# Kernel tuning notes

Measured on AMD Instinct MI355X. Metric: run time of the kernel, lower is better.

Reference implementation:

```python
import jax, jax.numpy as jnp
import numpy as np

N_HEAD = 16

def setup_inputs() -> dict:
    key = jax.random.key(0)
    ks = jax.random.split(key, 5)
    B, T, D = 2, 2048, 1024
    BN = 1024  # bottleneck_dim
    s = 0.02
    return {
        "x": jax.random.normal(ks[0], (B, T, D), dtype=jnp.float32),
        "w_qkv": jax.random.normal(ks[1], (3 * BN, D), dtype=jnp.float32) * s,
        "b_qkv": jax.random.normal(ks[2], (3 * BN,), dtype=jnp.float32) * s,
        "w_proj": jax.random.normal(ks[3], (D, BN), dtype=jnp.float32) * s,
        "b_proj": jax.random.normal(ks[4], (D,), dtype=jnp.float32) * s,
        "top_k": 64,
    }

def reference(x, w_qkv, b_qkv, w_proj, b_proj, top_k):
    B, T, D = x.shape
    H = N_HEAD
    BN = w_qkv.shape[0] // 3
    Dh = BN // H
    # qkv projection; torch Linear: y = x @ W^T + b
    qkv = (x @ w_qkv.T + b_qkv).reshape(B, T, 3, H, Dh)
    q = jnp.moveaxis(qkv[:, :, 0], 1, 2)  # (B,H,T,Dh)
    k = jnp.moveaxis(qkv[:, :, 1], 1, 2)
    v = jnp.moveaxis(qkv[:, :, 2], 1, 2)
    att = jnp.einsum('bhqd,bhkd->bhqk', q, k) * (1.0 / np.sqrt(Dh).astype(np.float32))
    # SparseK mask: keep only top-k scores per query row, mask rest before softmax
    topv = jax.lax.top_k(att, top_k)[0]          # (B,H,T,top_k)
    thresh = topv[..., -1:]                      # kth largest per row
    att = jnp.where(att >= thresh, att, -jnp.inf)
    att = jax.nn.softmax(att, axis=-1)
    y = jnp.einsum('bhqk,bhkd->bhqd', att, v)    # (B,H,T,Dh)
    y = y.transpose(0, 2, 1, 3).reshape(B, T, BN)
    return y @ w_proj.T + b_proj
```

## Files before the change

### kernel.cpp

```cpp
#include <hip/hip_runtime.h>
#include <hip/hip_bf16.h>
#include <math.h>

#define Bz 2
#define Tz 2048
#define Dz 1024
#define Hz 16
#define DHz 64
#define BNz 1024
#define TOPKz 64
#define QBLK 16
#define CAND_MAX 176
#define BAND 8e-5f
#define SLO  -20.0f
#define SBINW 0.15625f
#define SBINR 6.4f
#define LDSB 40
#define HSTR 257

typedef __attribute__((ext_vector_type(8))) short bf16x8;
typedef __attribute__((ext_vector_type(4))) short s16x4;
typedef __attribute__((ext_vector_type(4))) float f32x4;

__device__ __forceinline__ short f2bf(float f) {
  unsigned u = __float_as_uint(f);
  return (short)((u + 0x7FFFu + ((u >> 16) & 1u)) >> 16);
}
__device__ __forceinline__ float bf2f(short b) {
  return __uint_as_float(((unsigned)(unsigned short)b) << 16);
}
__device__ __forceinline__ unsigned f2s(float f) {
  unsigned u = __float_as_uint(f);
  return (u & 0x80000000u) ? ~u : (u | 0x80000000u);
}
__device__ __forceinline__ float s2f(unsigned u) {
  return __uint_as_float((u & 0x80000000u) ? (u & 0x7FFFFFFFu) : ~u);
}

__global__ __launch_bounds__(256) void split3(
    const float* __restrict__ in, short* __restrict__ hh,
    short* __restrict__ mm, short* __restrict__ ll, int n4)
{
  int i = blockIdx.x * 256 + threadIdx.x;
  if (i >= n4) return;
  float4 v = ((const float4*)in)[i];
  float vv[4] = {v.x, v.y, v.z, v.w};
  s16x4 h4, m4, l4;
#pragma unroll
  for (int e = 0; e < 4; ++e) {
    short h = f2bf(vv[e]);
    float r1 = vv[e] - bf2f(h);
    short m = f2bf(r1);
    float r2 = r1 - bf2f(m);
    h4[e] = h; m4[e] = m; l4[e] = f2bf(r2);
  }
  ((s16x4*)hh)[i] = h4;
  ((s16x4*)mm)[i] = m4;
  ((s16x4*)ll)[i] = l4;
}

__global__ __launch_bounds__(256) void qkv_gemm_v2(
    const short* __restrict__ Axh, const short* __restrict__ Axm,
    const short* __restrict__ Axl, const short* __restrict__ Bwh,
    const short* __restrict__ Bwm, const short* __restrict__ Bwl,
    const float* __restrict__ bias,
    float* __restrict__ q32, float* __restrict__ k32,
    short* __restrict__ kbf, float* __restrict__ v32)
{
  __shared__ __align__(16) short Ah[128][LDSB];
  __shared__ __align__(16) short Am[128][LDSB];
  __shared__ __align__(16) short Al[128][LDSB];
  __shared__ __align__(16) short Bh[64][LDSB];
  __shared__ __align__(16) short Bm[64][LDSB];
  __shared__ __align__(16) short Bl[64][LDSB];

  const int tid = threadIdx.x;
  const int lane = tid & 63, wid = tid >> 6;
  const int m0 = blockIdx.y * 128, n0 = blockIdx.x * 64;
  const int bcol = lane & 15, lgrp = lane >> 4;

  f32x4 acch[2][4], accl[2][4];
#pragma unroll
  for (int ms = 0; ms < 2; ++ms)
#pragma unroll
    for (int nt = 0; nt < 4; ++nt) {
      acch[ms][nt] = (f32x4){0.f, 0.f, 0.f, 0.f};
      accl[ms][nt] = (f32x4){0.f, 0.f, 0.f, 0.f};
    }

  const int arow = tid >> 1, ak = (tid & 1) * 16;
  const int brow = tid >> 2, bk = (tid & 3) * 8;
  const size_t aoff = (size_t)(m0 + arow) * Dz + ak;
  const size_t boff = (size_t)(n0 + brow) * Dz + bk;

  for (int kt = 0; kt < Dz; kt += 32) {
    bf16x8 ah0 = *(const bf16x8*)(Axh + aoff + kt);
    bf16x8 ah1 = *(const bf16x8*)(Axh + aoff + kt + 8);
    bf16x8 am0 = *(const bf16x8*)(Axm + aoff + kt);
    bf16x8 am1 = *(const bf16x8*)(Axm + aoff + kt + 8);
    bf16x8 al0 = *(const bf16x8*)(Axl + aoff + kt);
    bf16x8 al1 = *(const bf16x8*)(Axl + aoff + kt + 8);
    bf16x8 bh8 = *(const bf16x8*)(Bwh + boff + kt);
    bf16x8 bm8 = *(const bf16x8*)(Bwm + boff + kt);
    bf16x8 bl8 = *(const bf16x8*)(Bwl + boff + kt);
    __syncthreads();
    *(bf16x8*)&Ah[arow][ak] = ah0;  *(bf16x8*)&Ah[arow][ak+8] = ah1;
    *(bf16x8*)&Am[arow][ak] = am0;  *(bf16x8*)&Am[arow][ak+8] = am1;
    *(bf16x8*)&Al[arow][ak] = al0;  *(bf16x8*)&Al[arow][ak+8] = al1;
    *(bf16x8*)&Bh[brow][bk] = bh8;
    *(bf16x8*)&Bm[brow][bk] = bm8;
    *(bf16x8*)&Bl[brow][bk] = bl8;
    __syncthreads();

    bf16x8 ahf[2], amf[2], alf[2];
#pragma unroll
    for (int ms = 0; ms < 2; ++ms) {
      int rr = wid*32 + ms*16 + bcol;
      ahf[ms] = *(const bf16x8*)&Ah[rr][lgrp*8];
      amf[ms] = *(const bf16x8*)&Am[rr][lgrp*8];
      alf[ms] = *(const bf16x8*)&Al[rr][lgrp*8];
    }
#pragma unroll
    for (int nt = 0; nt < 4; ++nt) {
      int nr = nt*16 + bcol;
      bf16x8 bh = *(const bf16x8*)&Bh[nr][lgrp*8];
      bf16x8 bm = *(const bf16x8*)&Bm[nr][lgrp*8];
      bf16x8 bl = *(const bf16x8*)&Bl[nr][lgrp*8];
#pragma unroll
      for (int ms = 0; ms < 2; ++ms) {
        acch[ms][nt] = __builtin_amdgcn_mfma_f32_16x16x32_bf16(ahf[ms], bh, acch[ms][nt], 0, 0, 0);
        accl[ms][nt] = __builtin_amdgcn_mfma_f32_16x16x32_bf16(ahf[ms], bm, accl[ms][nt], 0, 0, 0);
        accl[ms][nt] = __builtin_amdgcn_mfma_f32_16x16x32_bf16(amf[ms], bh, accl[ms][nt], 0, 0, 0);
        accl[ms][nt] = __builtin_amdgcn_mfma_f32_16x16x32_bf16(amf[ms], bm, accl[ms][nt], 0, 0, 0);
        accl[ms][nt] = __builtin_amdgcn_mfma_f32_16x16x32_bf16(ahf[ms], bl, accl[ms][nt], 0, 0, 0);
        accl[ms][nt] = __builtin_amdgcn_mfma_f32_16x16x32_bf16(alf[ms], bh, accl[ms][nt], 0, 0, 0);
      }
    }
  }

#pragma unroll
  for (int ms = 0; ms < 2; ++ms)
#pragma unroll
    for (int nt = 0; nt < 4; ++nt)
#pragma unroll
      for (int rv = 0; rv < 4; ++rv) {
        int m = m0 + wid*32 + ms*16 + lgrp*4 + rv;
        int n = n0 + nt*16 + bcol;
        double val = (double)acch[ms][nt][rv] + (double)accl[ms][nt][rv] + (double)bias[n];
        int bb = m >> 11;
        int t = m & 2047;
        if (n < BNz) {
          int h = n >> 6, d = n & 63;
          q32[(((size_t)(bb*Hz + h))*Tz + t)*DHz + d] = (float)val;
        } else if (n < 2*BNz) {
          int h = (n - BNz) >> 6, d = n & 63;
          size_t bh = (size_t)(bb*Hz + h);
          float vf = (float)val;
          k32[(bh*Tz + t)*DHz + d] = vf;
          kbf[(bh*Tz + t)*DHz + d] = f2bf(vf);
        } else {
          int h = (n - 2*BNz) >> 6, d = n & 63;
          v32[(((size_t)(bb*Hz + h))*Tz + t)*DHz + d] = (float)val;
        }
      }
}

__global__ __launch_bounds__(256) void proj_gemm_v2(
    const short* __restrict__ Ayh, const short* __restrict__ Aym,
    const short* __restrict__ Ayl, const short* __restrict__ Bwh,
    const short* __restrict__ Bwm, const short* __restrict__ Bwl,
    const float* __restrict__ bias, float* __restrict__ out)
{
  __shared__ __align__(16) short Ah[128][LDSB];
  __shared__ __align__(16) short Am[128][LDSB];
  __shared__ __align__(16) short Al[128][LDSB];
  __shared__ __align__(16) short Bh[64][LDSB];
  __shared__ __align__(16) short Bm[64][LDSB];
  __shared__ __align__(16) short Bl[64][LDSB];

  const int tid = threadIdx.x;
  const int lane = tid & 63, wid = tid >> 6;
  const int m0 = blockIdx.y * 128, n0 = blockIdx.x * 64;
  const int bcol = lane & 15, lgrp = lane >> 4;

  f32x4 acch[2][4], accl[2][4];
#pragma unroll
  for (int ms = 0; ms < 2; ++ms)
#pragma unroll
    for (int nt = 0; nt < 4; ++nt) {
      acch[ms][nt] = (f32x4){0.f, 0.f, 0.f, 0.f};
      accl[ms][nt] = (f32x4){0.f, 0.f, 0.f, 0.f};
    }

  const int arow = tid >> 1, ak = (tid & 1) * 16;
  const int brow = tid >> 2, bk = (tid & 3) * 8;
  const size_t aoff = (size_t)(m0 + arow) * Dz + ak;
  const size_t boff = (size_t)(n0 + brow) * Dz + bk;

  for (int kt = 0; kt < Dz; kt += 32) {
    bf16x8 ah0 = *(const bf16x8*)(Ayh + aoff + kt);
    bf16x8 ah1 = *(const bf16x8*)(Ayh + aoff + kt + 8);
    bf16x8 am0 = *(const bf16x8*)(Aym + aoff + kt);
    bf16x8 am1 = *(const bf16x8*)(Aym + aoff + kt + 8);
    bf16x8 al0 = *(const bf16x8*)(Ayl + aoff + kt);
    bf16x8 al1 = *(const bf16x8*)(Ayl + aoff + kt + 8);
    bf16x8 bh8 = *(const bf16x8*)(Bwh + boff + kt);
    bf16x8 bm8 = *(const bf16x8*)(Bwm + boff + kt);
    bf16x8 bl8 = *(const bf16x8*)(Bwl + boff + kt);
    __syncthreads();
    *(bf16x8*)&Ah[arow][ak] = ah0;  *(bf16x8*)&Ah[arow][ak+8] = ah1;
    *(bf16x8*)&Am[arow][ak] = am0;  *(bf16x8*)&Am[arow][ak+8] = am1;
    *(bf16x8*)&Al[arow][ak] = al0;  *(bf16x8*)&Al[arow][ak+8] = al1;
    *(bf16x8*)&Bh[brow][bk] = bh8;
    *(bf16x8*)&Bm[brow][bk] = bm8;
    *(bf16x8*)&Bl[brow][bk] = bl8;
    __syncthreads();

    bf16x8 ahf[2], amf[2], alf[2];
#pragma unroll
    for (int ms = 0; ms < 2; ++ms) {
      int rr = wid*32 + ms*16 + bcol;
      ahf[ms] = *(const bf16x8*)&Ah[rr][lgrp*8];
      amf[ms] = *(const bf16x8*)&Am[rr][lgrp*8];
      alf[ms] = *(const bf16x8*)&Al[rr][lgrp*8];
    }
#pragma unroll
    for (int nt = 0; nt < 4; ++nt) {
      int nr = nt*16 + bcol;
      bf16x8 bh = *(const bf16x8*)&Bh[nr][lgrp*8];
      bf16x8 bm = *(const bf16x8*)&Bm[nr][lgrp*8];
      bf16x8 bl = *(const bf16x8*)&Bl[nr][lgrp*8];
#pragma unroll
      for (int ms = 0; ms < 2; ++ms) {
        acch[ms][nt] = __builtin_amdgcn_mfma_f32_16x16x32_bf16(ahf[ms], bh, acch[ms][nt], 0, 0, 0);
        accl[ms][nt] = __builtin_amdgcn_mfma_f32_16x16x32_bf16(ahf[ms], bm, accl[ms][nt], 0, 0, 0);
        accl[ms][nt] = __builtin_amdgcn_mfma_f32_16x16x32_bf16(amf[ms], bh, accl[ms][nt], 0, 0, 0);
        accl[ms][nt] = __builtin_amdgcn_mfma_f32_16x16x32_bf16(amf[ms], bm, accl[ms][nt], 0, 0, 0);
        accl[ms][nt] = __builtin_amdgcn_mfma_f32_16x16x32_bf16(ahf[ms], bl, accl[ms][nt], 0, 0, 0);
        accl[ms][nt] = __builtin_amdgcn_mfma_f32_16x16x32_bf16(alf[ms], bh, accl[ms][nt], 0, 0, 0);
      }
    }
  }

#pragma unroll
  for (int ms = 0; ms < 2; ++ms)
#pragma unroll
    for (int nt = 0; nt < 4; ++nt)
#pragma unroll
      for (int rv = 0; rv < 4; ++rv) {
        int m = m0 + wid*32 + ms*16 + lgrp*4 + rv;
        int n = n0 + nt*16 + bcol;
        out[(size_t)m * Dz + n] = (acch[ms][nt][rv] + accl[ms][nt][rv]) + bias[n];
      }
}

__global__ __launch_bounds__(256) void attn_topk(
    const float* __restrict__ q32g, const float* __restrict__ k32g,
    const short* __restrict__ kbfg, const float* __restrict__ v32,
    float* __restrict__ y)
{
  __shared__ float q_s[QBLK][DHz];
  __shared__ __align__(16) unsigned char ubuf[QBLK*CAND_MAX*6];
  __shared__ int bstar_s[QBLK];
  __shared__ int candcnt[QBLK];

  unsigned* hist = (unsigned*)ubuf;
  float* candv = (float*)ubuf;
  unsigned short* candidx = (unsigned short*)(ubuf + QBLK*CAND_MAX*4);

  const int tid = threadIdx.x;
  const int bid0 = blockIdx.x;
  const int bh_f = (bid0 & 7) + 8 * (bid0 >> 10);
  const int qbf = (bid0 >> 3) & 127;
  const int h = bh_f & 15;
  const int bb = bh_f >> 4;
  const size_t bh = (size_t)(bb * Hz + h);
  const float* qg = q32g + (bh * Tz + (size_t)qbf * QBLK) * DHz;
  const float* kg32 = k32g + bh * Tz * DHz;
  const short* kb = kbfg + bh * Tz * DHz;
  const float* vg = v32 + bh * Tz * DHz;

  if (tid < QBLK) candcnt[tid] = 0;
  for (int i = tid; i < QBLK*HSTR; i += 256) hist[i] = 0u;
  {
    int r = tid >> 4, d4 = (tid & 15) * 4;
    *(float4*)&q_s[r][d4] = *(const float4*)&qg[r*DHz + d4];
  }
  __syncthreads();

  const int lane = tid & 63;
  const int wid = tid >> 6;
  const int bcol = lane & 15;
  const int lgrp = lane >> 4;
  bf16x8 aF0, aF1;
#pragma unroll
  for (int e = 0; e < 8; ++e) {
    aF0[e] = f2bf(q_s[bcol][lgrp*8 + e]);
    aF1[e] = f2bf(q_s[bcol][32 + lgrp*8 + e]);
  }
  const int t0base = wid * 512;

  unsigned binreg[32];
#pragma unroll 4
  for (int tt = 0; tt < 32; ++tt) {
    const short* kbp = kb + (size_t)(t0base + tt*16 + bcol) * DHz;
    bf16x8 b0 = *(const bf16x8*)(kbp + lgrp*8);
    bf16x8 b1 = *(const bf16x8*)(kbp + 32 + lgrp*8);
    f32x4 c = {0.f, 0.f, 0.f, 0.f};
    c = __builtin_amdgcn_mfma_f32_16x16x32_bf16(aF0, b0, c, 0, 0, 0);
    c = __builtin_amdgcn_mfma_f32_16x16x32_bf16(aF1, b1, c, 0, 0, 0);
    unsigned bw = 0u;
#pragma unroll
    for (int j = 0; j < 4; ++j) {
      int bin = (int)((c[j] - SLO) * SBINR);
      bin = bin < 0 ? 0 : (bin > 255 ? 255 : bin);
      atomicAdd(&hist[(lgrp*4 + j)*HSTR + bin], 1u);
      bw |= ((unsigned)bin) << (8*j);
    }
    binreg[tt] = bw;
  }
  __syncthreads();

  {
    int r = tid >> 4, i16 = tid & 15;
    int s = 0;
#pragma unroll
    for (int j = 0; j < 16; ++j) s += (int)hist[r*HSTR + i16*16 + j];
    int S = s;
#pragma unroll
    for (int off = 1; off < 16; off <<= 1) {
      int src = i16 + off;
      int v = __shfl(S, (lane & 48) | (src < 16 ? src : 15));
      S += (src < 16) ? v : 0;
    }
    unsigned long long blt = __ballot(S >= TOPKz);
    unsigned mask16 = (unsigned)((blt >> (lane & 48)) & 0xFFFFull);
    int istar = 31 - __builtin_clz(mask16);
    if (i16 == istar) {
      int cum = S - s;
      int b = istar * 16;
      for (int j = 15; j >= 0; --j) {
        cum += (int)hist[r*HSTR + istar*16 + j];
        if (cum >= TOPKz) { b = istar*16 + j; break; }
      }
      bstar_s[r] = b;
    }
  }
  __syncthreads();

  {
    int bc[4];
#pragma unroll
    for (int j = 0; j < 4; ++j) {
      int b = bstar_s[lgrp*4 + j] - 1;
      bc[j] = b < 0 ? 0 : b;
    }
#pragma unroll
    for (int tt = 0; tt < 32; ++tt) {
      unsigned bw = binreg[tt];
#pragma unroll
      for (int j = 0; j < 4; ++j) {
        int bin = (int)((bw >> (8*j)) & 255u);
        if (bin >= bc[j]) {
          int r = lgrp*4 + j;
          int p = atomicAdd(&candcnt[r], 1);
          if (p < CAND_MAX) candidx[r*CAND_MAX + p] = (unsigned short)(t0base + tt*16 + bcol);
        }
      }
    }
  }
  __syncthreads();

  {
    const int r = tid >> 4, i16 = tid & 15;
    int n = candcnt[r]; if (n > CAND_MAX) n = CAND_MAX;

    for (int i = i16; i < n; i += 16) {
      int col = (int)candidx[r*CAND_MAX + i];
      const float* kpd = kg32 + (size_t)col * DHz;
      double s = 0.0;
#pragma unroll
      for (int d = 0; d < DHz; d += 4) {
        float4 k4 = *(const float4*)(kpd + d);
        s = fma((double)q_s[r][d+0], (double)k4.x, s);
        s = fma((double)q_s[r][d+1], (double)k4.y, s);
        s = fma((double)q_s[r][d+2], (double)k4.z, s);
        s = fma((double)q_s[r][d+3], (double)k4.w, s);
      }
      candv[r*CAND_MAX + i] = (float)s;
    }

    float myv[11];
    float mx = -3.0e38f;
#pragma unroll
    for (int j = 0; j < 11; ++j) {
      int i = i16 + j*16;
      float x = (i < n) ? candv[r*CAND_MAX + i] : -3.0e38f;
      myv[j] = x;
      mx = fmaxf(mx, x);
    }
#pragma unroll
    for (int m = 1; m < 16; m <<= 1) mx = fmaxf(mx, __shfl_xor(mx, m));

    float mn = 3.0e38f;
#pragma unroll
    for (int j = 0; j < 11; ++j) {
      int i = i16 + j*16;
      if (i < n) mn = fminf(mn, myv[j]);
    }
#pragma unroll
    for (int m = 1; m < 16; m <<= 1) mn = fminf(mn, __shfl_xor(mn, m));
    unsigned lo_u = f2s(mn);
    unsigned hi_u = f2s(mx) + 1u;
    while (hi_u - lo_u > 1u) {
      unsigned mid = lo_u + ((hi_u - lo_u) >> 1);
      float tv = s2f(mid);
      int cnt = 0;
#pragma unroll
      for (int j = 0; j < 11; ++j) cnt += (myv[j] >= tv) ? 1 : 0;
#pragma unroll
      for (int m = 1; m < 16; m <<= 1) cnt += __shfl_xor(cnt, m);
      if (cnt >= TOPKz) lo_u = mid; else hi_u = mid;
    }
    const float T = s2f(lo_u);

    int na = 0, nb = 0;
#pragma unroll
    for (int j = 0; j < 11; ++j) {
      float s = myv[j];
      if (s > T + BAND) na++;
      else if (s >= T - BAND) nb++;
    }
#pragma unroll
    for (int m = 1; m < 16; m <<= 1) {
      na += __shfl_xor(na, m);
      nb += __shfl_xor(nb, m);
    }
    const float wb = (float)(TOPKz - na) / (float)(nb > 0 ? nb : 1);

    float lsum = 0.f;
#pragma unroll
    for (int j = 0; j < 11; ++j) {
      int i = i16 + j*16;
      if (i < n) {
        float s = myv[j];
        float w = (s > T + BAND) ? 1.f : ((s >= T - BAND) ? wb : 0.f);
        float p = (w > 0.f) ? w * expf((s - mx) * 0.125f) : 0.f;
        candv[r*CAND_MAX + i] = p;
        lsum += p;
      }
    }
#pragma unroll
    for (int m = 1; m < 16; m <<= 1) lsum += __shfl_xor(lsum, m);
    const float rd = 1.0f / lsum;

    const int dg = i16 * 4;
    float4 o = make_float4(0.f, 0.f, 0.f, 0.f);
    for (int i = 0; i < n; ++i) {
      float p = candv[r*CAND_MAX + i];
      int idx = (int)candidx[r*CAND_MAX + i];
      float4 vv = *(const float4*)&vg[(size_t)idx*DHz + dg];
      float pw = p * rd;
      o.x = fmaf(pw, vv.x, o.x);
      o.y = fmaf(pw, vv.y, o.y);
      o.z = fmaf(pw, vv.z, o.z);
      o.w = fmaf(pw, vv.w, o.w);
    }
    float* yo = y + ((size_t)bb*Tz + (size_t)qbf*QBLK + r) * BNz + h*DHz + dg;
    *(float4*)yo = o;
  }
}

extern "C" void kernel_launch(void* const* d_in, const int* in_sizes, int n_in,
                              void* d_out, int out_size, void* d_ws, size_t ws_size,
                              hipStream_t stream)
{
  const float* x      = (const float*)d_in[0];
  const float* w_qkv  = (const float*)d_in[1];
  const float* b_qkv  = (const float*)d_in[2];
  const float* w_proj = (const float*)d_in[3];
  const float* b_proj = (const float*)d_in[4];
  float* out = (float*)d_out;

  const size_t E  = (size_t)Bz * Tz * Dz;
  const size_t Wq = (size_t)3 * BNz * Dz;
  const size_t Wp = (size_t)Dz * BNz;

  float* q32 = (float*)d_ws;
  float* k32 = q32 + E;
  short* kbf = (short*)(k32 + E);
  float* v32 = (float*)(kbf + E);
  float* y   = v32 + E;
  short* sAh = (short*)(y + E);
  short* sAm = sAh + E;
  short* sAl = sAm + E;
  short* sBh = sAl + E;
  short* sBm = sBh + Wq;
  short* sBl = sBm + Wq;

  split3<<<(int)(E/4/256), 256, 0, stream>>>(x, sAh, sAm, sAl, (int)(E/4));
  split3<<<(int)(Wq/4/256), 256, 0, stream>>>(w_qkv, sBh, sBm, sBl, (int)(Wq/4));
  qkv_gemm_v2<<<dim3((3*BNz)/64, (Bz*Tz)/128), 256, 0, stream>>>(
      sAh, sAm, sAl, sBh, sBm, sBl, b_qkv, q32, k32, kbf, v32);
  attn_topk<<<Bz*Hz*(Tz/QBLK), 256, 0, stream>>>(q32, k32, kbf, v32, y);
  split3<<<(int)(E/4/256), 256, 0, stream>>>(y, sAh, sAm, sAl, (int)(E/4));
  split3<<<(int)(Wp/4/256), 256, 0, stream>>>(w_proj, sBh, sBm, sBl, (int)(Wp/4));
  proj_gemm_v2<<<dim3(Dz/64, (Bz*Tz)/128), 256, 0, stream>>>(
      sAh, sAm, sAl, sBh, sBm, sBl, b_proj, out);
}
```

Before: 601.8 us.

## Replace LDS histogram threshold search with register-based binary search over bins

Drops the per-row 256-bin shared-memory histogram, which was built with atomic adds for every score, and its prefix-scan search for the top-k cutoff bin. Instead, each thread counts how many of its register-held bin values are at or above a midpoint, reduces the counts with shuffles plus a few LDS atomics, and narrows a per-row binary search over 8 iterations. This removes heavy LDS atomic contention but adds 16 block-wide barriers and repeated passes over the register-held bins.

```diff
diff --git a/kernel.cpp b/kernel.cpp
--- a/kernel.cpp
+++ b/kernel.cpp
@@ -16,7 +16,6 @@
 #define SBINW 0.15625f
 #define SBINR 6.4f
 #define LDSB 40
-#define HSTR 257
 
 typedef __attribute__((ext_vector_type(8))) short bf16x8;
 typedef __attribute__((ext_vector_type(4))) short s16x4;
@@ -261,10 +260,11 @@
 {
   __shared__ float q_s[QBLK][DHz];
   __shared__ __align__(16) unsigned char ubuf[QBLK*CAND_MAX*6];
+  __shared__ int rcnt[QBLK];
+  __shared__ int rlo[QBLK], rhi[QBLK], rmid[QBLK];
   __shared__ int bstar_s[QBLK];
   __shared__ int candcnt[QBLK];
 
-  unsigned* hist = (unsigned*)ubuf;
   float* candv = (float*)ubuf;
   unsigned short* candidx = (unsigned short*)(ubuf + QBLK*CAND_MAX*4);
 
@@ -280,8 +280,10 @@
   const short* kb = kbfg + bh * Tz * DHz;
   const float* vg = v32 + bh * Tz * DHz;
 
-  if (tid < QBLK) candcnt[tid] = 0;
-  for (int i = tid; i < QBLK*HSTR; i += 256) hist[i] = 0u;
+  if (tid < QBLK) {
+    candcnt[tid] = 0; rcnt[tid] = 0;
+    rlo[tid] = 0; rhi[tid] = 256; rmid[tid] = 128;
+  }
   {
     int r = tid >> 4, d4 = (tid & 15) * 4;
     *(float4*)&q_s[r][d4] = *(const float4*)&qg[r*DHz + d4];
@@ -314,38 +316,41 @@
     for (int j = 0; j < 4; ++j) {
       int bin = (int)((c[j] - SLO) * SBINR);
       bin = bin < 0 ? 0 : (bin > 255 ? 255 : bin);
-      atomicAdd(&hist[(lgrp*4 + j)*HSTR + bin], 1u);
       bw |= ((unsigned)bin) << (8*j);
     }
     binreg[tt] = bw;
   }
-  __syncthreads();
-
-  {
-    int r = tid >> 4, i16 = tid & 15;
-    int s = 0;
-#pragma unroll
-    for (int j = 0; j < 16; ++j) s += (int)hist[r*HSTR + i16*16 + j];
-    int S = s;
-#pragma unroll
-    for (int off = 1; off < 16; off <<= 1) {
-      int src = i16 + off;
-      int v = __shfl(S, (lane & 48) | (src < 16 ? src : 15));
-      S += (src < 16) ? v : 0;
-    }
-    unsigned long long blt = __ballot(S >= TOPKz);
-    unsigned mask16 = (unsigned)((blt >> (lane & 48)) & 0xFFFFull);
-    int istar = 31 - __builtin_clz(mask16);
-    if (i16 == istar) {
-      int cum = S - s;
-      int b = istar * 16;
-      for (int j = 15; j >= 0; --j) {
-        cum += (int)hist[r*HSTR + istar*16 + j];
-        if (cum >= TOPKz) { b = istar*16 + j; break; }
-      }
-      bstar_s[r] = b;
-    }
-  }
+
+#pragma unroll
+  for (int it = 0; it < 8; ++it) {
+    int bc[4];
+#pragma unroll
+    for (int j = 0; j < 4; ++j) bc[j] = rmid[lgrp*4 + j];
+    int cnt[4] = {0, 0, 0, 0};
+#pragma unroll
+    for (int tt = 0; tt < 32; ++tt) {
+      unsigned bw = binreg[tt];
+#pragma unroll
+      for (int j = 0; j < 4; ++j)
+        cnt[j] += ((int)((bw >> (8*j)) & 255u) >= bc[j]) ? 1 : 0;
+    }
+#pragma unroll
+    for (int m = 1; m < 16; m <<= 1)
+#pragma unroll
+      for (int j = 0; j < 4; ++j) cnt[j] += __shfl_xor(cnt[j], m);
+    if (bcol == 0) {
+#pragma unroll
+      for (int j = 0; j < 4; ++j) atomicAdd(&rcnt[lgrp*4 + j], cnt[j]);
+    }
+    __syncthreads();
+    if (tid < QBLK) {
+      int c = rcnt[tid]; rcnt[tid] = 0;
+      if (c >= TOPKz) rlo[tid] = rmid[tid]; else rhi[tid] = rmid[tid];
+      rmid[tid] = (rlo[tid] + rhi[tid]) >> 1;
+    }
+    __syncthreads();
+  }
+  if (tid < QBLK) bstar_s[tid] = rlo[tid];
   __syncthreads();
 
   {
```

Result: slower. 646.4 us (+7.4%).
